# Kernel tuning notes

Hardware: AMD Instinct MI355X
Metric: run time of the kernel (lower is better)

## Reference

```python
import jax, jax.numpy as jnp
import numpy as np

B, S, D, H = 4, 4096, 1024, 128

def setup_inputs() -> dict:
    key = jax.random.key(0)
    ks = jax.random.split(key, 4)
    scale = 1.0 / np.sqrt(D)
    return {
        "x":  jax.random.normal(ks[0], (B, S, D), dtype=jnp.float32),
        "Wq": jax.random.normal(ks[1], (D, H), dtype=jnp.float32) * scale,
        "bq": jnp.zeros((H,), dtype=jnp.float32),
        "Wk": jax.random.normal(ks[2], (D, H), dtype=jnp.float32) * scale,
        "bk": jnp.zeros((H,), dtype=jnp.float32),
        "Wv": jax.random.normal(ks[3], (D, H), dtype=jnp.float32) * scale,
        "bv": jnp.zeros((H,), dtype=jnp.float32),
    }

def reference(x, Wq, bq, Wk, bk, Wv, bv):
    # q, k, v: [B, S, H]
    q = x @ Wq + bq
    k = x @ Wk + bk
    v = x @ Wv + bv
    inv_sqrt_h = 1.0 / jnp.sqrt(jnp.asarray(q.shape[-1], q.dtype))
    # scores: [B, S, S]
    scores = jnp.einsum('bqh,bkh->bqk', q, k) * inv_sqrt_h
    seq = q.shape[1]
    causal = jnp.tril(jnp.ones((seq, seq), dtype=bool))
    scores = jnp.where(causal, scores, jnp.asarray(-jnp.inf, scores.dtype))
    probs = jax.nn.softmax(scores, axis=-1)
    # dropout p=0.0 -> identity
    return jnp.einsum('bqk,bkh->bqh', probs, v)
```

## Files before the change

kernel.cpp:

```cpp
#include <hip/hip_runtime.h>
#include <hip/hip_bf16.h>

#define B_ 4
#define S_ 4096
#define D_ 1024
#define H_ 128

typedef _Float16 half8 __attribute__((ext_vector_type(8)));
typedef _Float16 half4v __attribute__((ext_vector_type(4)));
typedef float float4v __attribute__((ext_vector_type(4)));


__device__ __forceinline__ void gload_lds16(const void* g, void* l) {
    __builtin_amdgcn_global_load_lds(
        (const __attribute__((address_space(1))) unsigned int*)g,
        (__attribute__((address_space(3))) unsigned int*)l, 16, 0, 0);
}

__global__ __launch_bounds__(256) void k_cvt_w(const float* __restrict__ Wq,
                                               const float* __restrict__ Wk,
                                               const float* __restrict__ Wv,
                                               _Float16* __restrict__ WT) {
    __shared__ _Float16 T[64][136];
    const float* W = blockIdx.y == 0 ? Wq : (blockIdx.y == 1 ? Wk : Wv);
    _Float16* WTw = WT + (size_t)blockIdx.y * (H_ * D_);
    const int k0 = blockIdx.x * 64;
    const int t  = threadIdx.x;

    const int r = t >> 2, c0 = (t & 3) * 32;
    const float* src = W + (size_t)(k0 + r) * H_ + c0;
#pragma unroll
    for (int c4 = 0; c4 < 8; ++c4) {
        float4v v = *(const float4v*)(src + c4 * 4);
        half4v h;
        h[0] = (_Float16)v[0]; h[1] = (_Float16)v[1];
        h[2] = (_Float16)v[2]; h[3] = (_Float16)v[3];
        *(half4v*)(&T[r][c0 + c4 * 4]) = h;
    }
    __syncthreads();

    const int n = t >> 1, ks = (t & 1) * 32;
#pragma unroll
    for (int c8 = 0; c8 < 4; ++c8) {
        half8 v;
#pragma unroll
        for (int e = 0; e < 8; ++e) v[e] = T[ks + c8 * 8 + e][n];
        *(half8*)(WTw + (size_t)n * D_ + k0 + ks + c8 * 8) = v;
    }
}

__global__ __launch_bounds__(256, 3) void k_proj(const float* __restrict__ X,
                                                 const _Float16* __restrict__ WT,
                                                 const float* __restrict__ bq,
                                                 const float* __restrict__ bk,
                                                 const float* __restrict__ bv,
                                                 _Float16* __restrict__ Qf,
                                                 _Float16* __restrict__ Kz,
                                                 _Float16* __restrict__ Vz) {
    __shared__ char smem[32768];
    char* AsB = smem;
    char* BsB = smem + 16384;

    const int t    = threadIdx.x;
    const int bid  = blockIdx.x;
    const int w    = bid >> 8;
    const int m0   = (bid & 255) * 64;
    const int lane = t & 63, wid = t >> 6;
    const int lo   = lane & 15, hi = lane >> 4;
    const int wr   = wid >> 1, wc = wid & 1;

    const _Float16* Wt = WT + (size_t)w * (H_ * D_);

    const int raj = wid * 16 + (lane >> 4);
    const int rbj = wid * 32 + (lane >> 3);
    const int ca0 = (lane & 15) * 4;
    const int cb0 = (lane & 7) * 8;

    float4v acc[2][4];
#pragma unroll
    for (int mt = 0; mt < 2; ++mt)
#pragma unroll
        for (int nt = 0; nt < 4; ++nt) acc[mt][nt] = {0.f, 0.f, 0.f, 0.f};

    for (int it = 0; it < 16; ++it) {
        const int k0 = it * 64;
#pragma unroll
        for (int j = 0; j < 4; ++j) {
            const int ra = raj + j * 4;
            const int ca = ca0 ^ ((ra & 7) * 4);
            gload_lds16(X + (size_t)(m0 + ra) * D_ + k0 + ca,
                        AsB + (wid * 16 + j * 4) * 256);
            const int rb = rbj + j * 8;
            const int cb = cb0 ^ ((rb & 7) * 8);
            gload_lds16(Wt + (size_t)rb * D_ + k0 + cb,
                        BsB + (wid * 32 + j * 8) * 128);
        }
        __syncthreads();
#pragma unroll
        for (int kk = 0; kk < 2; ++kk) {
            const int cb = kk * 32 + hi * 8;
            half8 af[2];
#pragma unroll
            for (int mt = 0; mt < 2; ++mt) {
                const int r = wr * 32 + mt * 16 + lo;
                const int v = (r & 7) * 4;
                float4v a0 = *(const float4v*)(AsB + r * 256 + ((cb ^ v) << 2));
                float4v a1 = *(const float4v*)(AsB + r * 256 + (((cb + 4) ^ v) << 2));
                half8 h;
                h[0]=(_Float16)a0[0]; h[1]=(_Float16)a0[1]; h[2]=(_Float16)a0[2]; h[3]=(_Float16)a0[3];
                h[4]=(_Float16)a1[0]; h[5]=(_Float16)a1[1]; h[6]=(_Float16)a1[2]; h[7]=(_Float16)a1[3];
                af[mt] = h;
            }
            half8 bf[4];
#pragma unroll
            for (int nt = 0; nt < 4; ++nt) {
                const int rb2 = wc * 64 + nt * 16 + lo;
                const int vb  = (rb2 & 7) * 8;
                bf[nt] = *(const half8*)(BsB + rb2 * 128 + (((cb) ^ vb) << 1));
            }
#pragma unroll
            for (int mt = 0; mt < 2; ++mt)
#pragma unroll
                for (int nt = 0; nt < 4; ++nt)
                    acc[mt][nt] = __builtin_amdgcn_mfma_f32_16x16x32_f16(
                        af[mt], bf[nt], acc[mt][nt], 0, 0, 0);
        }
        __syncthreads();
    }

    const float* bias = (w == 0) ? bq : ((w == 1) ? bk : bv);
    const float scale = (w == 0) ? (0.08838834764831845f * 1.4426950408889634f) : 1.0f;
    _Float16* Ct = (_Float16*)smem;
#pragma unroll
    for (int mt = 0; mt < 2; ++mt)
#pragma unroll
        for (int nt = 0; nt < 4; ++nt) {
            const int col   = wc * 64 + nt * 16 + lo;
            const float bn  = bias[col];
            const int rbase = wr * 32 + mt * 16 + 4 * hi;
#pragma unroll
            for (int j = 0; j < 4; ++j)
                Ct[(rbase + j) * 136 + col] = (_Float16)((acc[mt][nt][j] + bn) * scale);
        }
    __syncthreads();

    const int bb  = m0 >> 12;
    const int tt0 = (m0 & (S_ - 1)) >> 5;

    if (w == 0) {
        const int r = t >> 2, c0 = (t & 3) * 32;
        _Float16* dst = Qf + (size_t)(m0 + r) * H_ + c0;
        const _Float16* srcp = &Ct[r * 136 + c0];
#pragma unroll
        for (int cc = 0; cc < 4; ++cc)
            *(half8*)(dst + cc * 8) = *(const half8*)(srcp + cc * 8);
    } else if (w == 1) {
        const int rowp = ((lo >> 2) << 3) + (lo & 3);
#pragma unroll
        for (int q = 0; q < 4; ++q) {
            const int fid = wid * 4 + q;
            const int ft = fid >> 3, k2 = (fid >> 1) & 3, c = fid & 1;
            const int row = ft * 32 + rowp + 4 * c;
            half8 v = *(const half8*)(&Ct[row * 136 + k2 * 32 + hi * 8]);
            *(half8*)(Kz + (size_t)(bb * 128 + tt0 + ft) * 4096 +
                      (k2 * 2 + c) * 512 + lane * 8) = v;
        }
    } else {
#pragma unroll
        for (int q = 0; q < 4; ++q) {
            const int fid = wid * 4 + q;
            const int ft = fid >> 3, hc = fid & 7;
            half8 v;
#pragma unroll
            for (int e = 0; e < 8; ++e)
                v[e] = Ct[(ft * 32 + hi * 8 + e) * 136 + hc * 16 + lo];
            *(half8*)(Vz + (size_t)(bb * 128 + tt0 + ft) * 4096 +
                      hc * 512 + lane * 8) = v;
        }
    }
}

__global__ __launch_bounds__(512, 2) void k_attn(const _Float16* __restrict__ Qf,
                                                 const _Float16* __restrict__ Kz,
                                                 const _Float16* __restrict__ Vz,
                                                 float* __restrict__ Out) {
    __shared__ float    sm_l[8][32];
    __shared__ _Float16 sm_o[8][32][136];

    const int t    = threadIdx.x;
    const int lane = t & 63, wid = t >> 6;
    const int lo = lane & 15, hi = lane >> 4;

    const int i   = blockIdx.x;
    const int b   = (i >> 1) & 3;
    const int qtr = ((i >> 3) << 1) | (i & 1);
    const int qt  = (qtr < 64) ? qtr : (191 - qtr);
    const int q0  = qt << 5;

    const _Float16* Qb = Qf + (size_t)b * (S_ * H_);
    const _Float16* Kb = Kz + (size_t)b * 524288;
    const _Float16* Vb = Vz + (size_t)b * 524288;

    half8 qfa[4], qfb[4];
#pragma unroll
    for (int kk = 0; kk < 4; ++kk) {
        qfa[kk] = *(const half8*)(Qb + (size_t)(q0 + lo) * H_ + kk * 32 + hi * 8);
        qfb[kk] = *(const half8*)(Qb + (size_t)(q0 + 16 + lo) * H_ + kk * 32 + hi * 8);
    }

    float4v oa[8], ob[8];
#pragma unroll
    for (int hc = 0; hc < 8; ++hc) { oa[hc] = {0.f,0.f,0.f,0.f}; ob[hc] = {0.f,0.f,0.f,0.f}; }
    float la = 0.f, lb = 0.f;

    const int lane8 = lane * 8;
    const int ntiles = qt + 1;

    half8 kc0[4], kc1[4];
    if (wid < ntiles) {
        const _Float16* Kt = Kb + (size_t)wid * 4096 + lane8;
#pragma unroll
        for (int kk = 0; kk < 4; ++kk) {
            kc0[kk] = *(const half8*)(Kt + (kk * 2    ) * 512);
            kc1[kk] = *(const half8*)(Kt + (kk * 2 + 1) * 512);
        }
    }

    for (int tt = wid; tt < ntiles; tt += 8) {
        const _Float16* Vt = Vb + (size_t)tt * 4096 + lane8;
        half8 vf[8];
#pragma unroll
        for (int hc = 0; hc < 8; ++hc)
            vf[hc] = *(const half8*)(Vt + hc * 512);
        const int tn = (tt + 8 < ntiles) ? (tt + 8) : tt;
        half8 kn0[4], kn1[4];
        {
            const _Float16* Ktn = Kb + (size_t)tn * 4096 + lane8;
#pragma unroll
            for (int kk = 0; kk < 4; ++kk) {
                kn0[kk] = *(const half8*)(Ktn + (kk * 2    ) * 512);
                kn1[kk] = *(const half8*)(Ktn + (kk * 2 + 1) * 512);
            }
        }
        float4v s0a = {0.f,0.f,0.f,0.f}, s1a = {0.f,0.f,0.f,0.f};
        float4v s0b = {0.f,0.f,0.f,0.f}, s1b = {0.f,0.f,0.f,0.f};
        __builtin_amdgcn_s_setprio(1);
#pragma unroll
        for (int kk = 0; kk < 4; ++kk) {
            s0a = __builtin_amdgcn_mfma_f32_16x16x32_f16(kc0[kk], qfa[kk], s0a, 0, 0, 0);
            s0b = __builtin_amdgcn_mfma_f32_16x16x32_f16(kc0[kk], qfb[kk], s0b, 0, 0, 0);
            s1a = __builtin_amdgcn_mfma_f32_16x16x32_f16(kc1[kk], qfa[kk], s1a, 0, 0, 0);
            s1b = __builtin_amdgcn_mfma_f32_16x16x32_f16(kc1[kk], qfb[kk], s1b, 0, 0, 0);
        }
        __builtin_amdgcn_s_setprio(0);
        if (tt == qt) {
#pragma unroll
            for (int j = 0; j < 4; ++j) {
                const int c0 = 8 * hi + j, c1 = 8 * hi + 4 + j;
                if (c0 > lo)      s0a[j] = -INFINITY;
                if (c1 > lo)      s1a[j] = -INFINITY;
                if (c0 > 16 + lo) s0b[j] = -INFINITY;
                if (c1 > 16 + lo) s1b[j] = -INFINITY;
            }
        }
        float pa0 = __builtin_amdgcn_exp2f(s0a[0]), pa1 = __builtin_amdgcn_exp2f(s0a[1]);
        float pa2 = __builtin_amdgcn_exp2f(s0a[2]), pa3 = __builtin_amdgcn_exp2f(s0a[3]);
        float pa4 = __builtin_amdgcn_exp2f(s1a[0]), pa5 = __builtin_amdgcn_exp2f(s1a[1]);
        float pa6 = __builtin_amdgcn_exp2f(s1a[2]), pa7 = __builtin_amdgcn_exp2f(s1a[3]);
        float pb0 = __builtin_amdgcn_exp2f(s0b[0]), pb1 = __builtin_amdgcn_exp2f(s0b[1]);
        float pb2 = __builtin_amdgcn_exp2f(s0b[2]), pb3 = __builtin_amdgcn_exp2f(s0b[3]);
        float pb4 = __builtin_amdgcn_exp2f(s1b[0]), pb5 = __builtin_amdgcn_exp2f(s1b[1]);
        float pb6 = __builtin_amdgcn_exp2f(s1b[2]), pb7 = __builtin_amdgcn_exp2f(s1b[3]);
        la += ((pa0+pa1)+(pa2+pa3)) + ((pa4+pa5)+(pa6+pa7));
        lb += ((pb0+pb1)+(pb2+pb3)) + ((pb4+pb5)+(pb6+pb7));
        half8 pfa, pfb;
        pfa[0]=(_Float16)pa0; pfa[1]=(_Float16)pa1; pfa[2]=(_Float16)pa2; pfa[3]=(_Float16)pa3;
        pfa[4]=(_Float16)pa4; pfa[5]=(_Float16)pa5; pfa[6]=(_Float16)pa6; pfa[7]=(_Float16)pa7;
        pfb[0]=(_Float16)pb0; pfb[1]=(_Float16)pb1; pfb[2]=(_Float16)pb2; pfb[3]=(_Float16)pb3;
        pfb[4]=(_Float16)pb4; pfb[5]=(_Float16)pb5; pfb[6]=(_Float16)pb6; pfb[7]=(_Float16)pb7;
        __builtin_amdgcn_s_setprio(1);
#pragma unroll
        for (int hc = 0; hc < 8; ++hc) {
            oa[hc] = __builtin_amdgcn_mfma_f32_16x16x32_f16(vf[hc], pfa, oa[hc], 0, 0, 0);
            ob[hc] = __builtin_amdgcn_mfma_f32_16x16x32_f16(vf[hc], pfb, ob[hc], 0, 0, 0);
        }
        __builtin_amdgcn_s_setprio(0);
#pragma unroll
        for (int kk = 0; kk < 4; ++kk) { kc0[kk] = kn0[kk]; kc1[kk] = kn1[kk]; }
    }

    la += __shfl_xor(la, 16); la += __shfl_xor(la, 32);
    lb += __shfl_xor(lb, 16); lb += __shfl_xor(lb, 32);

    sm_l[wid][lo]      = la;
    sm_l[wid][16 + lo] = lb;
#pragma unroll
    for (int hc = 0; hc < 8; ++hc) {
        half4v va, vb;
#pragma unroll
        for (int j = 0; j < 4; ++j) { va[j] = (_Float16)oa[hc][j]; vb[j] = (_Float16)ob[hc][j]; }
        *(half4v*)(&sm_o[wid][lo][hc * 16 + 4 * hi])      = va;
        *(half4v*)(&sm_o[wid][16 + lo][hc * 16 + 4 * hi]) = vb;
    }
    __syncthreads();

#pragma unroll
    for (int qh = 0; qh < 2; ++qh) {
        const int q = qh * 16 + lo;
        float L = 0.f;
#pragma unroll
        for (int w = 0; w < 8; ++w) L += sm_l[w][q];
        const float invL = 1.f / L;
        float4v ov = {0.f, 0.f, 0.f, 0.f};
#pragma unroll
        for (int w = 0; w < 8; ++w) {
            half4v tv = *(const half4v*)(&sm_o[w][q][wid * 16 + 4 * hi]);
#pragma unroll
            for (int j = 0; j < 4; ++j) ov[j] += (float)tv[j];
        }
#pragma unroll
        for (int j = 0; j < 4; ++j) ov[j] *= invL;
        *(float4v*)(Out + ((size_t)b * S_ + q0 + q) * H_ + wid * 16 + 4 * hi) = ov;
    }
}

extern "C" void kernel_launch(void* const* d_in, const int* in_sizes, int n_in,
                              void* d_out, int out_size, void* d_ws, size_t ws_size,
                              hipStream_t stream) {
    const float* x  = (const float*)d_in[0];
    const float* Wq = (const float*)d_in[1];
    const float* bq = (const float*)d_in[2];
    const float* Wk = (const float*)d_in[3];
    const float* bk = (const float*)d_in[4];
    const float* Wv = (const float*)d_in[5];
    const float* bv = (const float*)d_in[6];
    float* out = (float*)d_out;

    char* ws = (char*)d_ws;
    _Float16* WT = (_Float16*)ws;
    _Float16* Qf = (_Float16*)(ws + 786432);
    _Float16* Kz = (_Float16*)(ws + 786432 + 4194304);
    _Float16* Vz = (_Float16*)(ws + 786432 + 8388608);

    hipLaunchKernelGGL(k_cvt_w, dim3(16, 3), dim3(256), 0, stream, Wq, Wk, Wv, WT);
    hipLaunchKernelGGL(k_proj, dim3(768), dim3(256), 0, stream,
                       x, WT, bq, bk, bv, Qf, Kz, Vz);
    hipLaunchKernelGGL(k_attn, dim3(512), dim3(512), 0, stream, Qf, Kz, Vz, out);
}
```

Measured before the change: 61.64 us.

## Triple-buffer projection GEMM LDS stages with async prefetch and vmcnt waits

Rewrites the projection kernel's K loop from a single 64-wide stage with two barriers per iteration into a 3-buffer pipeline of 32-wide K stages. Two stages are prefetched ahead via global_load_lds, and each iteration waits with a partial vmcnt and one barrier. This is meant to overlap global-to-LDS traffic with MFMA work and halve barrier count per K element. LDS use grows from 32KB to 48KB, which may reduce occupancy at the 3-blocks-per-CU launch bound, and there are twice as many loop iterations.

```diff
diff --git a/kernel.cpp b/kernel.cpp
--- a/kernel.cpp
+++ b/kernel.cpp
@@ -57,9 +57,7 @@
                                                  _Float16* __restrict__ Qf,
                                                  _Float16* __restrict__ Kz,
                                                  _Float16* __restrict__ Vz) {
-    __shared__ char smem[32768];
-    char* AsB = smem;
-    char* BsB = smem + 16384;
+    __shared__ char smem[49152];
 
     const int t    = threadIdx.x;
     const int bid  = blockIdx.x;
@@ -71,10 +69,27 @@
 
     const _Float16* Wt = WT + (size_t)w * (H_ * D_);
 
-    const int raj = wid * 16 + (lane >> 4);
-    const int rbj = wid * 32 + (lane >> 3);
-    const int ca0 = (lane & 15) * 4;
-    const int cb0 = (lane & 7) * 8;
+    const int la3 = lane >> 3, la7 = lane & 7;
+    const int lb2 = lane >> 2, lb3 = lane & 3;
+
+#define STAGE(buf, s)                                                          \
+    {                                                                          \
+        char* base = smem + (buf) * 16384;                                     \
+        const int k0s = (s) * 32;                                              \
+        _Pragma("unroll")                                                      \
+        for (int j = 0; j < 2; ++j) {                                          \
+            const int ai = wid * 2 + j;                   \
+            const int ra = ai * 8 + la3;                                       \
+            const int ca = (la7 * 4) ^ ((ra & 7) * 4);                         \
+            gload_lds16(X + (size_t)(m0 + ra) * D_ + k0s + ca,                 \
+                        base + ai * 1024);                                     \
+            const int bi = wid * 2 + j;                 \
+            const int rb = bi * 16 + lb2;                                      \
+            const int cb = (lb3 * 8) ^ ((rb & 3) * 8);                         \
+            gload_lds16(Wt + (size_t)rb * D_ + k0s + cb,                       \
+                        base + 8192 + bi * 1024);                              \
+        }                                                                      \
+    }
 
     float4v acc[2][4];
 #pragma unroll
@@ -82,51 +97,51 @@
 #pragma unroll
         for (int nt = 0; nt < 4; ++nt) acc[mt][nt] = {0.f, 0.f, 0.f, 0.f};
 
-    for (int it = 0; it < 16; ++it) {
-        const int k0 = it * 64;
-#pragma unroll
-        for (int j = 0; j < 4; ++j) {
-            const int ra = raj + j * 4;
-            const int ca = ca0 ^ ((ra & 7) * 4);
-            gload_lds16(X + (size_t)(m0 + ra) * D_ + k0 + ca,
-                        AsB + (wid * 16 + j * 4) * 256);
-            const int rb = rbj + j * 8;
-            const int cb = cb0 ^ ((rb & 7) * 8);
-            gload_lds16(Wt + (size_t)rb * D_ + k0 + cb,
-                        BsB + (wid * 32 + j * 8) * 128);
-        }
-        __syncthreads();
-#pragma unroll
-        for (int kk = 0; kk < 2; ++kk) {
-            const int cb = kk * 32 + hi * 8;
-            half8 af[2];
-#pragma unroll
-            for (int mt = 0; mt < 2; ++mt) {
-                const int r = wr * 32 + mt * 16 + lo;
-                const int v = (r & 7) * 4;
-                float4v a0 = *(const float4v*)(AsB + r * 256 + ((cb ^ v) << 2));
-                float4v a1 = *(const float4v*)(AsB + r * 256 + (((cb + 4) ^ v) << 2));
-                half8 h;
-                h[0]=(_Float16)a0[0]; h[1]=(_Float16)a0[1]; h[2]=(_Float16)a0[2]; h[3]=(_Float16)a0[3];
-                h[4]=(_Float16)a1[0]; h[5]=(_Float16)a1[1]; h[6]=(_Float16)a1[2]; h[7]=(_Float16)a1[3];
-                af[mt] = h;
-            }
-            half8 bf[4];
-#pragma unroll
-            for (int nt = 0; nt < 4; ++nt) {
-                const int rb2 = wc * 64 + nt * 16 + lo;
-                const int vb  = (rb2 & 7) * 8;
-                bf[nt] = *(const half8*)(BsB + rb2 * 128 + (((cb) ^ vb) << 1));
-            }
-#pragma unroll
-            for (int mt = 0; mt < 2; ++mt)
-#pragma unroll
-                for (int nt = 0; nt < 4; ++nt)
-                    acc[mt][nt] = __builtin_amdgcn_mfma_f32_16x16x32_f16(
-                        af[mt], bf[nt], acc[mt][nt], 0, 0, 0);
-        }
-        __syncthreads();
-    }
+    STAGE(0, 0);
+    STAGE(1, 1);
+
+    for (int s = 0; s < 32; ++s) {
+        if (s < 31) {
+            asm volatile("s_waitcnt vmcnt(4)" ::: "memory");
+        } else {
+            asm volatile("s_waitcnt vmcnt(0)" ::: "memory");
+        }
+        __builtin_amdgcn_sched_barrier(0);
+        __builtin_amdgcn_s_barrier();
+        if (s < 30) STAGE((s + 2) % 3, s + 2);
+
+        const char* AsB = smem + (s % 3) * 16384;
+        const char* BsB = AsB + 8192;
+        const int c0 = hi * 8;
+        half8 af[2];
+#pragma unroll
+        for (int mt = 0; mt < 2; ++mt) {
+            const int r = wr * 32 + mt * 16 + lo;
+            const int v = (r & 7) * 4;
+            float4v a0 = *(const float4v*)(AsB + r * 128 + ((c0 ^ v) << 2));
+            float4v a1 = *(const float4v*)(AsB + r * 128 + (((c0 + 4) ^ v) << 2));
+            half8 h;
+            h[0]=(_Float16)a0[0]; h[1]=(_Float16)a0[1]; h[2]=(_Float16)a0[2]; h[3]=(_Float16)a0[3];
+            h[4]=(_Float16)a1[0]; h[5]=(_Float16)a1[1]; h[6]=(_Float16)a1[2]; h[7]=(_Float16)a1[3];
+            af[mt] = h;
+        }
+        half8 bf[4];
+#pragma unroll
+        for (int nt = 0; nt < 4; ++nt) {
+            const int rb2 = wc * 64 + nt * 16 + lo;
+            const int vb  = (rb2 & 3) * 8;
+            bf[nt] = *(const half8*)(BsB + rb2 * 64 + ((c0 ^ vb) << 1));
+        }
+#pragma unroll
+        for (int mt = 0; mt < 2; ++mt)
+#pragma unroll
+            for (int nt = 0; nt < 4; ++nt)
+                acc[mt][nt] = __builtin_amdgcn_mfma_f32_16x16x32_f16(
+                    af[mt], bf[nt], acc[mt][nt], 0, 0, 0);
+    }
+#undef STAGE
+
+    __syncthreads();
 
     const float* bias = (w == 0) ? bq : ((w == 1) ? bk : bv);
     const float scale = (w == 0) ? (0.08838834764831845f * 1.4426950408889634f) : 1.0f;
@@ -148,9 +163,9 @@
     const int tt0 = (m0 & (S_ - 1)) >> 5;
 
     if (w == 0) {
-        const int r = t >> 2, c0 = (t & 3) * 32;
-        _Float16* dst = Qf + (size_t)(m0 + r) * H_ + c0;
-        const _Float16* srcp = &Ct[r * 136 + c0];
+        const int r = t >> 2, c0q = (t & 3) * 32;
+        _Float16* dst = Qf + (size_t)(m0 + r) * H_ + c0q;
+        const _Float16* srcp = &Ct[r * 136 + c0q];
 #pragma unroll
         for (int cc = 0; cc < 4; ++cc)
             *(half8*)(dst + cc * 8) = *(const half8*)(srcp + cc * 8);
```

After: 66.38 us. 7.7% more time.

## Fuse Q/K/V projections into one block computing all 384 output columns

Applied to the files above, without the earlier changes.

Each projection block now computes Q, K and V for its 64-row tile, covering all 384 output columns, instead of launching separate blocks per weight matrix. The X tile is loaded and converted to fp16 once rather than three times, which cuts global reads of the fp32 input threefold. In exchange the grid shrinks from 768 to 256 blocks, with larger per-thread accumulators, 64KB of LDS and one block per CU. This lowers occupancy and latency hiding on a 256-CU-class GPU.

```diff
diff --git a/kernel.cpp b/kernel.cpp
--- a/kernel.cpp
+++ b/kernel.cpp
@@ -49,7 +49,7 @@
     }
 }
 
-__global__ __launch_bounds__(256, 3) void k_proj(const float* __restrict__ X,
+__global__ __launch_bounds__(256, 1) void k_proj(const float* __restrict__ X,
                                                  const _Float16* __restrict__ WT,
                                                  const float* __restrict__ bq,
                                                  const float* __restrict__ bk,
@@ -57,30 +57,25 @@
                                                  _Float16* __restrict__ Qf,
                                                  _Float16* __restrict__ Kz,
                                                  _Float16* __restrict__ Vz) {
-    __shared__ char smem[32768];
+    __shared__ char smem[65536];
     char* AsB = smem;
     char* BsB = smem + 16384;
 
     const int t    = threadIdx.x;
-    const int bid  = blockIdx.x;
-    const int w    = bid >> 8;
-    const int m0   = (bid & 255) * 64;
+    const int m0   = blockIdx.x * 64;
     const int lane = t & 63, wid = t >> 6;
     const int lo   = lane & 15, hi = lane >> 4;
-    const int wr   = wid >> 1, wc = wid & 1;
-
-    const _Float16* Wt = WT + (size_t)w * (H_ * D_);
 
     const int raj = wid * 16 + (lane >> 4);
-    const int rbj = wid * 32 + (lane >> 3);
     const int ca0 = (lane & 15) * 4;
+    const int rbs = lane >> 3;
     const int cb0 = (lane & 7) * 8;
 
-    float4v acc[2][4];
-#pragma unroll
-    for (int mt = 0; mt < 2; ++mt)
-#pragma unroll
-        for (int nt = 0; nt < 4; ++nt) acc[mt][nt] = {0.f, 0.f, 0.f, 0.f};
+    float4v acc[4][6];
+#pragma unroll
+    for (int mt = 0; mt < 4; ++mt)
+#pragma unroll
+        for (int nt = 0; nt < 6; ++nt) acc[mt][nt] = {0.f, 0.f, 0.f, 0.f};
 
     for (int it = 0; it < 16; ++it) {
         const int k0 = it * 64;
@@ -90,82 +85,92 @@
             const int ca = ca0 ^ ((ra & 7) * 4);
             gload_lds16(X + (size_t)(m0 + ra) * D_ + k0 + ca,
                         AsB + (wid * 16 + j * 4) * 256);
-            const int rb = rbj + j * 8;
+        }
+#pragma unroll
+        for (int j = 0; j < 12; ++j) {
+            const int bi = wid * 12 + j;
+            const int rb = bi * 8 + rbs;
             const int cb = cb0 ^ ((rb & 7) * 8);
-            gload_lds16(Wt + (size_t)rb * D_ + k0 + cb,
-                        BsB + (wid * 32 + j * 8) * 128);
+            gload_lds16(WT + (size_t)rb * D_ + k0 + cb,
+                        BsB + bi * 1024);
         }
         __syncthreads();
 #pragma unroll
         for (int kk = 0; kk < 2; ++kk) {
-            const int cb = kk * 32 + hi * 8;
-            half8 af[2];
-#pragma unroll
-            for (int mt = 0; mt < 2; ++mt) {
-                const int r = wr * 32 + mt * 16 + lo;
+            const int cbk = kk * 32 + hi * 8;
+            half8 af[4];
+#pragma unroll
+            for (int mt = 0; mt < 4; ++mt) {
+                const int r = mt * 16 + lo;
                 const int v = (r & 7) * 4;
-                float4v a0 = *(const float4v*)(AsB + r * 256 + ((cb ^ v) << 2));
-                float4v a1 = *(const float4v*)(AsB + r * 256 + (((cb + 4) ^ v) << 2));
+                float4v a0 = *(const float4v*)(AsB + r * 256 + ((cbk ^ v) << 2));
+                float4v a1 = *(const float4v*)(AsB + r * 256 + (((cbk + 4) ^ v) << 2));
                 half8 h;
                 h[0]=(_Float16)a0[0]; h[1]=(_Float16)a0[1]; h[2]=(_Float16)a0[2]; h[3]=(_Float16)a0[3];
                 h[4]=(_Float16)a1[0]; h[5]=(_Float16)a1[1]; h[6]=(_Float16)a1[2]; h[7]=(_Float16)a1[3];
                 af[mt] = h;
             }
-            half8 bf[4];
-#pragma unroll
-            for (int nt = 0; nt < 4; ++nt) {
-                const int rb2 = wc * 64 + nt * 16 + lo;
+            half8 bf[6];
+#pragma unroll
+            for (int nt = 0; nt < 6; ++nt) {
+                const int rb2 = wid * 96 + nt * 16 + lo;
                 const int vb  = (rb2 & 7) * 8;
-                bf[nt] = *(const half8*)(BsB + rb2 * 128 + (((cb) ^ vb) << 1));
+                bf[nt] = *(const half8*)(BsB + rb2 * 128 + ((cbk ^ vb) << 1));
             }
 #pragma unroll
-            for (int mt = 0; mt < 2; ++mt)
-#pragma unroll
-                for (int nt = 0; nt < 4; ++nt)
+            for (int mt = 0; mt < 4; ++mt)
+#pragma unroll
+                for (int nt = 0; nt < 6; ++nt)
                     acc[mt][nt] = __builtin_amdgcn_mfma_f32_16x16x32_f16(
                         af[mt], bf[nt], acc[mt][nt], 0, 0, 0);
         }
         __syncthreads();
     }
 
-    const float* bias = (w == 0) ? bq : ((w == 1) ? bk : bv);
-    const float scale = (w == 0) ? (0.08838834764831845f * 1.4426950408889634f) : 1.0f;
+    const float qsc = 0.08838834764831845f * 1.4426950408889634f;
     _Float16* Ct = (_Float16*)smem;
 #pragma unroll
-    for (int mt = 0; mt < 2; ++mt)
-#pragma unroll
-        for (int nt = 0; nt < 4; ++nt) {
-            const int col   = wc * 64 + nt * 16 + lo;
-            const float bn  = bias[col];
-            const int rbase = wr * 32 + mt * 16 + 4 * hi;
+    for (int nt = 0; nt < 6; ++nt) {
+        const int ng = wid * 96 + nt * 16;
+        const int wsel = ng >> 7;
+        const float* bp = (wsel == 0) ? bq : ((wsel == 1) ? bk : bv);
+        const float bn  = bp[(ng & 127) + lo];
+        const float sc  = (wsel == 0) ? qsc : 1.0f;
+        const int col   = ng + lo;
+#pragma unroll
+        for (int mt = 0; mt < 4; ++mt) {
+            const int rbase = mt * 16 + 4 * hi;
 #pragma unroll
             for (int j = 0; j < 4; ++j)
-                Ct[(rbase + j) * 136 + col] = (_Float16)((acc[mt][nt][j] + bn) * scale);
-        }
+                Ct[(rbase + j) * 392 + col] = (_Float16)((acc[mt][nt][j] + bn) * sc);
+        }
+    }
     __syncthreads();
 
     const int bb  = m0 >> 12;
     const int tt0 = (m0 & (S_ - 1)) >> 5;
 
-    if (w == 0) {
-        const int r = t >> 2, c0 = (t & 3) * 32;
-        _Float16* dst = Qf + (size_t)(m0 + r) * H_ + c0;
-        const _Float16* srcp = &Ct[r * 136 + c0];
+    {
+        const int r = t >> 2, c0q = (t & 3) * 32;
+        _Float16* dst = Qf + (size_t)(m0 + r) * H_ + c0q;
+        const _Float16* srcp = &Ct[r * 392 + c0q];
 #pragma unroll
         for (int cc = 0; cc < 4; ++cc)
             *(half8*)(dst + cc * 8) = *(const half8*)(srcp + cc * 8);
-    } else if (w == 1) {
+    }
+    {
         const int rowp = ((lo >> 2) << 3) + (lo & 3);
 #pragma unroll
         for (int q = 0; q < 4; ++q) {
             const int fid = wid * 4 + q;
             const int ft = fid >> 3, k2 = (fid >> 1) & 3, c = fid & 1;
             const int row = ft * 32 + rowp + 4 * c;
-            half8 v = *(const half8*)(&Ct[row * 136 + k2 * 32 + hi * 8]);
+            half8 v = *(const half8*)(&Ct[row * 392 + 128 + k2 * 32 + hi * 8]);
             *(half8*)(Kz + (size_t)(bb * 128 + tt0 + ft) * 4096 +
                       (k2 * 2 + c) * 512 + lane * 8) = v;
         }
-    } else {
+    }
+    {
 #pragma unroll
         for (int q = 0; q < 4; ++q) {
             const int fid = wid * 4 + q;
@@ -173,7 +178,7 @@
             half8 v;
 #pragma unroll
             for (int e = 0; e < 8; ++e)
-                v[e] = Ct[(ft * 32 + hi * 8 + e) * 136 + hc * 16 + lo];
+                v[e] = Ct[(ft * 32 + hi * 8 + e) * 392 + 256 + hc * 16 + lo];
             *(half8*)(Vz + (size_t)(bb * 128 + tt0 + ft) * 4096 +
                       hc * 512 + lane * 8) = v;
         }
@@ -343,7 +348,7 @@
     _Float16* Vz = (_Float16*)(ws + 786432 + 8388608);
 
     hipLaunchKernelGGL(k_cvt_w, dim3(16, 3), dim3(256), 0, stream, Wq, Wk, Wv, WT);
-    hipLaunchKernelGGL(k_proj, dim3(768), dim3(256), 0, stream,
+    hipLaunchKernelGGL(k_proj, dim3(256), dim3(256), 0, stream,
                        x, WT, bq, bk, bv, Qf, Kz, Vz);
     hipLaunchKernelGGL(k_attn, dim3(512), dim3(512), 0, stream, Qf, Kz, Vz, out);
 }
```

Measured after the change: 77.03 us. +25.0%, slower.
